# Performance work log

Hardware: AMD Instinct MI355X
Metric: run time of the kernel (lower is better)

Reference implementation:

```python
import jax, jax.numpy as jnp
import numpy as np

NHEAD = 4
HEAD_DIM = 64  # att_features per head = atten_feats // nhead


def setup_inputs() -> dict:
    key = jax.random.key(0)
    ks = jax.random.split(key, 8)
    N, D = 8192, 256
    s = 1.0 / np.sqrt(D)
    return {
        "x": jax.random.normal(ks[0], (N, D), dtype=jnp.float32),
        "edge": jax.random.randint(ks[1], (N, N), 0, 2, dtype=jnp.int32),
        "Wq": jax.random.normal(ks[2], (D, D), dtype=jnp.float32) * s,
        "bq": jax.random.normal(ks[3], (D,), dtype=jnp.float32) * 0.01,
        "Wk": jax.random.normal(ks[4], (D, D), dtype=jnp.float32) * s,
        "bk": jax.random.normal(ks[5], (D,), dtype=jnp.float32) * 0.01,
        "Wv": jax.random.normal(ks[6], (D, D), dtype=jnp.float32) * s,
        "bv": jax.random.normal(ks[7], (D,), dtype=jnp.float32) * 0.01,
    }


def _split_heads(t):
    # (N, H*d) -> (H, N, d)
    N = t.shape[0]
    return t.reshape(N, NHEAD, HEAD_DIM).transpose(1, 0, 2)


def reference(x, edge, Wq, bq, Wk, bk, Wv, bv):
    q = _split_heads(x @ Wq + bq)  # (H, N, d)
    k = _split_heads(x @ Wk + bk)
    v = _split_heads(x @ Wv + bv)
    # additive graph mask: 0 where edge.T == 1, -10000 where edge.T == 0
    mask = (edge.T.astype(jnp.float32) - 1.0) * 10000.0  # (N, N)
    scores = jnp.einsum("hnd,hmd->hnm", q, k) / np.sqrt(HEAD_DIM)
    scores = scores + mask[None, :, :]
    attn = jax.nn.softmax(scores, axis=-1)  # dropout is identity at eval
    ctx = jnp.einsum("hnm,hmd->hnd", attn, v)
    # (H, N, d) -> (N, H*d)
    return ctx.transpose(1, 0, 2).reshape(x.shape[0], NHEAD * HEAD_DIM)
```

## Files before the change

kernel.cpp:

```cpp
#include <hip/hip_runtime.h>
#include <stdint.h>

typedef unsigned short u16;
typedef unsigned int u32;
typedef unsigned long long u64;

typedef __attribute__((ext_vector_type(8))) __bf16 bf16x8;
typedef __attribute__((ext_vector_type(4))) float f32x4;

#define NROW 8192
#define DMODEL 256
#define HD 64
#define LDT 72

__device__ __forceinline__ u16 f2bf(float f) {
    u32 u = __builtin_bit_cast(u32, f);
    u += 0x7FFFu + ((u >> 16) & 1u);
    return (u16)(u >> 16);
}
__device__ __forceinline__ bf16x8 ldb8(const u16* p) {
    uint4 v = *(const uint4*)p;
    return __builtin_bit_cast(bf16x8, v);
}
__device__ __forceinline__ f32x4 mfma16(bf16x8 a, bf16x8 b, f32x4 c) {
    return __builtin_amdgcn_mfma_f32_16x16x32_bf16(a, b, c, 0, 0, 0);
}

__global__ __launch_bounds__(256) void k_prep(
    const float* __restrict__ x,
    const float* __restrict__ Wq, const float* __restrict__ Wk,
    const float* __restrict__ Wv,
    u16* __restrict__ xb, u16* __restrict__ Wt) {
    const int t = threadIdx.x;
    if (blockIdx.x < 1024) {
        size_t idx = (size_t)blockIdx.x * 2048 + t * 8;
        f32x4 a = *(const f32x4*)&x[idx];
        f32x4 b = *(const f32x4*)&x[idx + 4];
        uint4 o;
        o.x = (u32)f2bf(a[0]) | ((u32)f2bf(a[1]) << 16);
        o.y = (u32)f2bf(a[2]) | ((u32)f2bf(a[3]) << 16);
        o.z = (u32)f2bf(b[0]) | ((u32)f2bf(b[1]) << 16);
        o.w = (u32)f2bf(b[2]) | ((u32)f2bf(b[3]) << 16);
        *(uint4*)&xb[idx] = o;
        return;
    }
    __shared__ __align__(16) u16 lw[64 * LDT];
    int wb = blockIdx.x - 1024;
    int mat = wb >> 4, tile = wb & 15;
    int k0 = (tile >> 2) * 64, n0 = (tile & 3) * 64;
    const float* W = (mat == 0) ? Wq : ((mat == 1) ? Wk : Wv);
    #pragma unroll
    for (int i = 0; i < 4; ++i) {
        int c = t + 256 * i;
        int k = c >> 4, c4 = c & 15;
        f32x4 w4 = *(const f32x4*)&W[(size_t)(k0 + k) * DMODEL + n0 + c4 * 4];
        uint2 pk;
        pk.x = (u32)f2bf(w4[0]) | ((u32)f2bf(w4[1]) << 16);
        pk.y = (u32)f2bf(w4[2]) | ((u32)f2bf(w4[3]) << 16);
        *(uint2*)&lw[k * LDT + c4 * 4] = pk;
    }
    __syncthreads();
    #pragma unroll
    for (int i = 0; i < 2; ++i) {
        int c = t + 256 * i;
        int n = c >> 3, k8 = c & 7;
        union { uint4 u; u16 s[8]; } pk;
        #pragma unroll
        for (int j = 0; j < 8; ++j) pk.s[j] = lw[(k8 * 8 + j) * LDT + n];
        *(uint4*)&Wt[(size_t)mat * 65536 + (size_t)(n0 + n) * DMODEL + k0 + k8 * 8] = pk.u;
    }
}

__global__ __launch_bounds__(256) void k_bitmask(const int* __restrict__ edge,
                                                 u64* __restrict__ bits) {
    __shared__ u64 lb[8][128];
    const int t = threadIdx.x;
    const int lane = t & 63, w = t >> 6;
    const u32 m8 = blockIdx.x * 8u;
    #pragma unroll
    for (int rr = 0; rr < 2; ++rr) {
        const int mloc = w * 2 + rr;
        const size_t base = (size_t)(m8 + mloc) * NROW;
        for (int nwb = 0; nwb < 128; nwb += 16) {
            int v[16];
            #pragma unroll
            for (int j = 0; j < 16; ++j)
                v[j] = edge[base + (size_t)(nwb + j) * 64 + lane];
            u64 b[16];
            #pragma unroll
            for (int j = 0; j < 16; ++j) b[j] = __ballot(v[j] != 0);
            if (lane == 0) {
                #pragma unroll
                for (int j = 0; j < 16; ++j) lb[mloc][nwb + j] = b[j];
            }
        }
    }
    __syncthreads();
    const int nw = t >> 1, mh = (t & 1) * 4;
    u64 a0 = lb[mh + 0][nw], a1 = lb[mh + 1][nw];
    u64 a2 = lb[mh + 2][nw], a3 = lb[mh + 3][nw];
    u64* dst = &bits[(size_t)nw * NROW + m8 + mh];
    uint4 p0, p1;
    p0.x = (u32)a0; p0.y = (u32)(a0 >> 32); p0.z = (u32)a1; p0.w = (u32)(a1 >> 32);
    p1.x = (u32)a2; p1.y = (u32)(a2 >> 32); p1.z = (u32)a3; p1.w = (u32)(a3 >> 32);
    *(uint4*)dst = p0;
    *(uint4*)(dst + 2) = p1;
}

__global__ __launch_bounds__(256, 3) void k_qkv(
    const u16* __restrict__ xb, const u16* __restrict__ Wt,
    const float* __restrict__ bq, const float* __restrict__ bk,
    const float* __restrict__ bv,
    u16* __restrict__ Qo, u16* __restrict__ Ko, u16* __restrict__ Vt) {
    __shared__ __align__(16) u16 ax[128 * LDT];
    __shared__ __align__(16) u16 wt[64 * LDT];
    const int t = threadIdx.x;
    const int lane = t & 63, wv = t >> 6;
    const int q4 = lane >> 4, l15 = lane & 15;
    const int wr = wv >> 1, wc = wv & 1;
    const int row0 = blockIdx.x * 128;
    const int mat = blockIdx.y >> 2;
    const int c0 = (blockIdx.y & 3) * 64;
    const u16* Wm = Wt + (size_t)mat * 65536;
    const float* bias = (mat == 0) ? bq : ((mat == 1) ? bk : bv);

    f32x4 acc[8];
    #pragma unroll
    for (int i = 0; i < 8; ++i) acc[i] = {0.f, 0.f, 0.f, 0.f};

    for (int kk = 0; kk < DMODEL; kk += 64) {
        #pragma unroll
        for (int i = 0; i < 4; ++i) {
            int c = t + 256 * i;
            int row = c >> 3, c8 = c & 7;
            *(uint4*)&ax[row * LDT + c8 * 8] =
                *(const uint4*)&xb[(size_t)(row0 + row) * DMODEL + kk + c8 * 8];
        }
        #pragma unroll
        for (int i = 0; i < 2; ++i) {
            int c = t + 256 * i;
            int n = c >> 3, c8 = c & 7;
            *(uint4*)&wt[n * LDT + c8 * 8] =
                *(const uint4*)&Wm[(size_t)(c0 + n) * DMODEL + kk + c8 * 8];
        }
        __syncthreads();
        #pragma unroll
        for (int ks = 0; ks < 2; ++ks) {
            bf16x8 xf[4], wf[2];
            #pragma unroll
            for (int it = 0; it < 4; ++it)
                xf[it] = ldb8(&ax[(wr * 64 + it * 16 + l15) * LDT + ks * 32 + q4 * 8]);
            #pragma unroll
            for (int jt = 0; jt < 2; ++jt)
                wf[jt] = ldb8(&wt[(wc * 32 + jt * 16 + l15) * LDT + ks * 32 + q4 * 8]);
            if (mat < 2) {
                #pragma unroll
                for (int it = 0; it < 4; ++it)
                    #pragma unroll
                    for (int jt = 0; jt < 2; ++jt)
                        acc[it * 2 + jt] = mfma16(xf[it], wf[jt], acc[it * 2 + jt]);
            } else {
                #pragma unroll
                for (int jt = 0; jt < 2; ++jt)
                    #pragma unroll
                    for (int it = 0; it < 4; ++it)
                        acc[jt * 4 + it] = mfma16(wf[jt], xf[it], acc[jt * 4 + it]);
            }
        }
        __syncthreads();
    }

    if (mat < 2) {
        u16* out = (mat == 0) ? Qo : Ko;
        const float scale = (mat == 0) ? 0.18033688f : 1.0f;
        #pragma unroll
        for (int jt = 0; jt < 2; ++jt) {
            int col = c0 + wc * 32 + jt * 16 + l15;
            float bcol = bias[col];
            #pragma unroll
            for (int it = 0; it < 4; ++it) {
                int rowb = row0 + wr * 64 + it * 16 + q4 * 4;
                f32x4 a = acc[it * 2 + jt];
                #pragma unroll
                for (int r = 0; r < 4; ++r)
                    out[(size_t)(rowb + r) * DMODEL + col] = f2bf((a[r] + bcol) * scale);
            }
        }
    } else {
        #pragma unroll
        for (int jt = 0; jt < 2; ++jt) {
            #pragma unroll
            for (int r = 0; r < 4; ++r) {
                int drow = c0 + wc * 32 + jt * 16 + q4 * 4 + r;
                float bd = bias[drow];
                #pragma unroll
                for (int it = 0; it < 4; ++it) {
                    int col = row0 + wr * 64 + it * 16 + l15;
                    Vt[(size_t)drow * NROW + col] = f2bf(acc[jt * 4 + it][r] + bd);
                }
            }
        }
    }
}

__global__ __launch_bounds__(256, 2) void k_attn(
    const u16* __restrict__ Q, const u16* __restrict__ K,
    const u16* __restrict__ Vt, const u64* __restrict__ bits,
    float* __restrict__ out) {
    __shared__ __align__(16) u16 sK[2][64 * 64];
    __shared__ __align__(16) u16 sV[2][64 * 64];
    __shared__ __align__(16) u16 sP[4][16 * 64];
    __shared__ __align__(16) u32 sB[2][2][64];

    const int t = threadIdx.x;
    const int lane = t & 63, w = t >> 6;
    const int q4 = lane >> 4, l15 = lane & 15;
    const int l7 = l15 & 7;
    const int bid = blockIdx.x;
    const int h = (bid >> 1) & 3;
    const int qt = ((bid >> 3) << 1) | (bid & 1);
    const int n0 = qt * 64;
    const int half = w >> 1;
    const u32 shift = (u32)((w & 1) * 16 + l15);
    const int sr = t >> 3, sc = t & 7;
    const int ssw = (sc ^ (sr & 7)) * 8;

    bf16x8 qf[2];
    #pragma unroll
    for (int ks = 0; ks < 2; ++ks)
        qf[ks] = ldb8(&Q[(size_t)(n0 + w * 16 + l15) * DMODEL + h * HD + ks * 32 + q4 * 8]);

    uint4 onesu = {0x3F803F80u, 0x3F803F80u, 0x3F803F80u, 0x3F803F80u};
    const bf16x8 ones = __builtin_bit_cast(bf16x8, onesu);

    f32x4 o[4], lacc;
    lacc = {0.f, 0.f, 0.f, 0.f};
    #pragma unroll
    for (int dt = 0; dt < 4; ++dt) o[dt] = {0.f, 0.f, 0.f, 0.f};

    uint4 rk0, rk1, rv0, rv1; uint2 rb;
    {
        rk0 = *(const uint4*)&K[(size_t)(0 + sr) * DMODEL + h * HD + sc * 8];
        rk1 = *(const uint4*)&K[(size_t)(32 + sr) * DMODEL + h * HD + sc * 8];
        rv0 = *(const uint4*)&Vt[(size_t)(h * HD + sr) * NROW + 0 + sc * 8];
        rv1 = *(const uint4*)&Vt[(size_t)(h * HD + 32 + sr) * NROW + 0 + sc * 8];
        if (t < 64) rb = *(const uint2*)&bits[(size_t)qt * NROW + 0 + t];
        *(uint4*)&sK[0][sr * 64 + ssw] = rk0;
        *(uint4*)&sK[0][(32 + sr) * 64 + ssw] = rk1;
        *(uint4*)&sV[0][sr * 64 + ssw] = rv0;
        *(uint4*)&sV[0][(32 + sr) * 64 + ssw] = rv1;
        if (t < 64) { sB[0][0][t] = rb.x; sB[0][1][t] = rb.y; }
    }

    for (int kt = 0; kt < 128; ++kt) {
        __syncthreads();
        const int buf = kt & 1;
        if (kt < 127) {
            int m0 = (kt + 1) * 64;
            rk0 = *(const uint4*)&K[(size_t)(m0 + sr) * DMODEL + h * HD + sc * 8];
            rk1 = *(const uint4*)&K[(size_t)(m0 + 32 + sr) * DMODEL + h * HD + sc * 8];
            rv0 = *(const uint4*)&Vt[(size_t)(h * HD + sr) * NROW + m0 + sc * 8];
            rv1 = *(const uint4*)&Vt[(size_t)(h * HD + 32 + sr) * NROW + m0 + sc * 8];
            if (t < 64) rb = *(const uint2*)&bits[(size_t)qt * NROW + m0 + t];
        }

        f32x4 s[4];
        #pragma unroll
        for (int tj = 0; tj < 4; ++tj) s[tj] = {0.f, 0.f, 0.f, 0.f};
        #pragma unroll
        for (int ks = 0; ks < 2; ++ks) {
            bf16x8 kb[4];
            #pragma unroll
            for (int tj = 0; tj < 4; ++tj)
                kb[tj] = ldb8(&sK[buf][(tj * 16 + l15) * 64 + (((ks * 4 + q4) ^ l7) * 8)]);
            #pragma unroll
            for (int tj = 0; tj < 4; ++tj)
                s[tj] = mfma16(kb[tj], qf[ks], s[tj]);
        }

        #pragma unroll
        for (int tj = 0; tj < 4; ++tj) {
            uint4 bw = *(const uint4*)&sB[buf][half][tj * 16 + q4 * 4];
            u32 wd[4] = {bw.x, bw.y, bw.z, bw.w};
            u32 ub[4];
            #pragma unroll
            for (int r = 0; r < 4; ++r) {
                float sv = ((wd[r] >> shift) & 1u) ? s[tj][r] : -1e30f;
                ub[r] = __builtin_bit_cast(u32, __builtin_amdgcn_exp2f(sv));
            }
            uint2 pk;
            pk.x = (ub[0] >> 16) | (ub[1] & 0xFFFF0000u);
            pk.y = (ub[2] >> 16) | (ub[3] & 0xFFFF0000u);
            *(uint2*)&sP[w][l15 * 64 + (((tj * 2 + (q4 >> 1)) ^ l7) * 8) + (q4 & 1) * 4] = pk;
        }
        asm volatile("s_waitcnt lgkmcnt(0)" ::: "memory");

        #pragma unroll
        for (int ks = 0; ks < 2; ++ks) {
            bf16x8 pf = ldb8(&sP[w][l15 * 64 + (((ks * 4 + q4) ^ l7) * 8)]);
            bf16x8 vb[4];
            #pragma unroll
            for (int dt = 0; dt < 4; ++dt)
                vb[dt] = ldb8(&sV[buf][(dt * 16 + l15) * 64 + (((ks * 4 + q4) ^ l7) * 8)]);
            #pragma unroll
            for (int dt = 0; dt < 4; ++dt)
                o[dt] = mfma16(pf, vb[dt], o[dt]);
            lacc = mfma16(pf, ones, lacc);
        }

        if (kt < 127) {
            const int nb = buf ^ 1;
            *(uint4*)&sK[nb][sr * 64 + ssw] = rk0;
            *(uint4*)&sK[nb][(32 + sr) * 64 + ssw] = rk1;
            *(uint4*)&sV[nb][sr * 64 + ssw] = rv0;
            *(uint4*)&sV[nb][(32 + sr) * 64 + ssw] = rv1;
            if (t < 64) { sB[nb][0][t] = rb.x; sB[nb][1][t] = rb.y; }
        }
    }

    #pragma unroll
    for (int r = 0; r < 4; ++r) {
        float inv = __builtin_amdgcn_rcpf(lacc[r] + 1e-30f);
        int n = n0 + w * 16 + q4 * 4 + r;
        #pragma unroll
        for (int dt = 0; dt < 4; ++dt)
            out[(size_t)n * DMODEL + h * HD + dt * 16 + l15] = o[dt][r] * inv;
    }
}

extern "C" void kernel_launch(void* const* d_in, const int* in_sizes, int n_in,
                              void* d_out, int out_size, void* d_ws, size_t ws_size,
                              hipStream_t stream) {
    const float* x  = (const float*)d_in[0];
    const int* edge = (const int*)d_in[1];
    const float* Wq = (const float*)d_in[2];
    const float* bq = (const float*)d_in[3];
    const float* Wk = (const float*)d_in[4];
    const float* bk = (const float*)d_in[5];
    const float* Wv = (const float*)d_in[6];
    const float* bv = (const float*)d_in[7];

    char* ws = (char*)d_ws;
    u64* bits = (u64*)ws;
    u16* Qo  = (u16*)(ws + (8u << 20));
    u16* Ko  = (u16*)(ws + (12u << 20));
    u16* Vt  = (u16*)(ws + (16u << 20));
    u16* xb  = (u16*)(ws + (20u << 20));
    u16* Wt  = (u16*)(ws + (24u << 20));
    float* out = (float*)d_out;

    hipLaunchKernelGGL(k_prep, dim3(1072), dim3(256), 0, stream, x, Wq, Wk, Wv, xb, Wt);
    hipLaunchKernelGGL(k_bitmask, dim3(1024), dim3(256), 0, stream, edge, bits);
    hipLaunchKernelGGL(k_qkv, dim3(64, 12), dim3(256), 0, stream,
                       xb, Wt, bq, bk, bv, Qo, Ko, Vt);
    hipLaunchKernelGGL(k_attn, dim3(512), dim3(256), 0, stream, Qo, Ko, Vt, bits, out);
}
```

Baseline: 516.9 us.

## Split attention key dimension into four slices with separate reduction kernel

The attention kernel now splits the 8192 keys into four slices of 2048, launching 2048 blocks instead of 512. Each block writes unnormalized partial outputs and row sums to a workspace, and a new reduce kernel sums the slices, normalizes, and transposes into the output. This is meant to fix under-occupancy: 512 blocks is too few to fill the GPU's compute units. The cost is an extra launch plus partial-result traffic through global memory. Skipping the max subtraction stays valid across slices because the sums are purely additive.

```diff
diff --git a/kernel.cpp b/kernel.cpp
--- a/kernel.cpp
+++ b/kernel.cpp
@@ -206,7 +206,7 @@
 __global__ __launch_bounds__(256, 2) void k_attn(
     const u16* __restrict__ Q, const u16* __restrict__ K,
     const u16* __restrict__ Vt, const u64* __restrict__ bits,
-    float* __restrict__ out) {
+    float* __restrict__ po) {
     __shared__ __align__(16) u16 sK[2][64 * 64];
     __shared__ __align__(16) u16 sV[2][64 * 64];
     __shared__ __align__(16) u16 sP[4][16 * 64];
@@ -217,9 +217,12 @@
     const int q4 = lane >> 4, l15 = lane & 15;
     const int l7 = l15 & 7;
     const int bid = blockIdx.x;
-    const int h = (bid >> 1) & 3;
-    const int qt = ((bid >> 3) << 1) | (bid & 1);
+    const int sl = bid >> 9;
+    const int b9 = bid & 511;
+    const int h = (b9 >> 1) & 3;
+    const int qt = ((b9 >> 3) << 1) | (b9 & 1);
     const int n0 = qt * 64;
+    const int mbase = sl * 2048;
     const int half = w >> 1;
     const u32 shift = (u32)((w & 1) * 16 + l15);
     const int sr = t >> 3, sc = t & 7;
@@ -240,11 +243,11 @@
 
     uint4 rk0, rk1, rv0, rv1; uint2 rb;
     {
-        rk0 = *(const uint4*)&K[(size_t)(0 + sr) * DMODEL + h * HD + sc * 8];
-        rk1 = *(const uint4*)&K[(size_t)(32 + sr) * DMODEL + h * HD + sc * 8];
-        rv0 = *(const uint4*)&Vt[(size_t)(h * HD + sr) * NROW + 0 + sc * 8];
-        rv1 = *(const uint4*)&Vt[(size_t)(h * HD + 32 + sr) * NROW + 0 + sc * 8];
-        if (t < 64) rb = *(const uint2*)&bits[(size_t)qt * NROW + 0 + t];
+        rk0 = *(const uint4*)&K[(size_t)(mbase + sr) * DMODEL + h * HD + sc * 8];
+        rk1 = *(const uint4*)&K[(size_t)(mbase + 32 + sr) * DMODEL + h * HD + sc * 8];
+        rv0 = *(const uint4*)&Vt[(size_t)(h * HD + sr) * NROW + mbase + sc * 8];
+        rv1 = *(const uint4*)&Vt[(size_t)(h * HD + 32 + sr) * NROW + mbase + sc * 8];
+        if (t < 64) rb = *(const uint2*)&bits[(size_t)qt * NROW + mbase + t];
         *(uint4*)&sK[0][sr * 64 + ssw] = rk0;
         *(uint4*)&sK[0][(32 + sr) * 64 + ssw] = rk1;
         *(uint4*)&sV[0][sr * 64 + ssw] = rv0;
@@ -252,11 +255,11 @@
         if (t < 64) { sB[0][0][t] = rb.x; sB[0][1][t] = rb.y; }
     }
 
-    for (int kt = 0; kt < 128; ++kt) {
+    for (int it = 0; it < 32; ++it) {
         __syncthreads();
-        const int buf = kt & 1;
-        if (kt < 127) {
-            int m0 = (kt + 1) * 64;
+        const int buf = it & 1;
+        if (it < 31) {
+            int m0 = mbase + (it + 1) * 64;
             rk0 = *(const uint4*)&K[(size_t)(m0 + sr) * DMODEL + h * HD + sc * 8];
             rk1 = *(const uint4*)&K[(size_t)(m0 + 32 + sr) * DMODEL + h * HD + sc * 8];
             rv0 = *(const uint4*)&Vt[(size_t)(h * HD + sr) * NROW + m0 + sc * 8];
@@ -308,7 +311,7 @@
             lacc = mfma16(pf, ones, lacc);
         }
 
-        if (kt < 127) {
+        if (it < 31) {
             const int nb = buf ^ 1;
             *(uint4*)&sK[nb][sr * 64 + ssw] = rk0;
             *(uint4*)&sK[nb][(32 + sr) * 64 + ssw] = rk1;
@@ -318,13 +321,54 @@
         }
     }
 
-    #pragma unroll
-    for (int r = 0; r < 4; ++r) {
-        float inv = __builtin_amdgcn_rcpf(lacc[r] + 1e-30f);
-        int n = n0 + w * 16 + q4 * 4 + r;
-        #pragma unroll
-        for (int dt = 0; dt < 4; ++dt)
-            out[(size_t)n * DMODEL + h * HD + dt * 16 + l15] = o[dt][r] * inv;
+    float* pob = po + (size_t)bid * 4160;
+    #pragma unroll
+    for (int dt = 0; dt < 4; ++dt)
+        *(f32x4*)&pob[(dt * 16 + l15) * 64 + w * 16 + q4 * 4] = o[dt];
+    if (l15 == 0) {
+        #pragma unroll
+        for (int r = 0; r < 4; ++r) pob[4096 + w * 16 + q4 * 4 + r] = lacc[r];
+    }
+}
+
+__global__ __launch_bounds__(256) void k_reduce(const float* __restrict__ po,
+                                                float* __restrict__ out) {
+    __shared__ float sT[64 * 68];
+    __shared__ float sL[64];
+    const int t = threadIdx.x;
+    const int b9 = blockIdx.x;
+    const int h = (b9 >> 1) & 3;
+    const int qt = ((b9 >> 3) << 1) | (b9 & 1);
+    const int n0 = qt * 64;
+    const size_t base = (size_t)b9 * 4160;
+    const int d = t >> 2, ng = (t & 3) * 16;
+    f32x4 a[4];
+    #pragma unroll
+    for (int j = 0; j < 4; ++j) a[j] = {0.f, 0.f, 0.f, 0.f};
+    #pragma unroll
+    for (int s = 0; s < 4; ++s) {
+        const float* p = po + base + (size_t)s * (512 * 4160) + d * 64 + ng;
+        #pragma unroll
+        for (int j = 0; j < 4; ++j) a[j] += *(const f32x4*)&p[j * 4];
+    }
+    #pragma unroll
+    for (int j = 0; j < 4; ++j) *(f32x4*)&sT[d * 68 + ng + j * 4] = a[j];
+    if (t < 64) {
+        float l = 0.f;
+        #pragma unroll
+        for (int s = 0; s < 4; ++s) l += po[base + (size_t)s * (512 * 4160) + 4096 + t];
+        sL[t] = l;
+    }
+    __syncthreads();
+    const int n = t >> 2, dg = (t & 3) * 16;
+    float inv = __builtin_amdgcn_rcpf(sL[n] + 1e-30f);
+    #pragma unroll
+    for (int j = 0; j < 4; ++j) {
+        f32x4 v;
+        #pragma unroll
+        for (int i = 0; i < 4; ++i) v[i] = sT[(dg + j * 4 + i) * 68 + n];
+        v = v * inv;
+        *(f32x4*)&out[(size_t)(n0 + n) * DMODEL + h * HD + dg + j * 4] = v;
     }
 }
 
@@ -347,11 +391,13 @@
     u16* Vt  = (u16*)(ws + (16u << 20));
     u16* xb  = (u16*)(ws + (20u << 20));
     u16* Wt  = (u16*)(ws + (24u << 20));
+    float* po = (float*)(ws + (32u << 20));
     float* out = (float*)d_out;
 
     hipLaunchKernelGGL(k_prep, dim3(1072), dim3(256), 0, stream, x, Wq, Wk, Wv, xb, Wt);
     hipLaunchKernelGGL(k_bitmask, dim3(1024), dim3(256), 0, stream, edge, bits);
     hipLaunchKernelGGL(k_qkv, dim3(64, 12), dim3(256), 0, stream,
                        xb, Wt, bq, bk, bv, Qo, Ko, Vt);
-    hipLaunchKernelGGL(k_attn, dim3(512), dim3(256), 0, stream, Qo, Ko, Vt, bits, out);
-}
+    hipLaunchKernelGGL(k_attn, dim3(2048), dim3(256), 0, stream, Qo, Ko, Vt, bits, po);
+    hipLaunchKernelGGL(k_reduce, dim3(512), dim3(256), 0, stream, po, out);
+}
```

Measured after the change: 514.4 us. Within noise of the previous version (-0.5%).
